# Kernel tuning notes

Measured on AMD Instinct MI355X. Metric: run time of the kernel, lower is better.

Reference implementation:

```python
import jax, jax.numpy as jnp
import numpy as np

E, H, D, T, B = 768, 12, 64, 2048, 2
HID = 4 * E

def _layernorm(x, g, b, eps=1e-5):
    mu = jnp.mean(x, axis=-1, keepdims=True)
    var = jnp.mean(jnp.square(x - mu), axis=-1, keepdims=True)
    return (x - mu) * jax.lax.rsqrt(var + eps) * g + b

def setup_inputs() -> dict:
    key = jax.random.key(0)
    ks = jax.random.split(key, 8)
    s = 0.02
    return {
        "x": jax.random.normal(ks[0], (B, T, E), jnp.float32),
        "Wq": jax.random.normal(ks[1], (H, E, D), jnp.float32) * s,
        "Wk": jax.random.normal(ks[2], (H, E, D), jnp.float32) * s,
        "Wv": jax.random.normal(ks[3], (H, E, D), jnp.float32) * s,
        "W1": jax.random.normal(ks[4], (E, HID), jnp.float32) * s,
        "b1": jnp.zeros((HID,), jnp.float32),
        "W2": jax.random.normal(ks[5], (HID, E), jnp.float32) * s,
        "b2": jnp.zeros((E,), jnp.float32),
        "ln1_g": jnp.ones((E,), jnp.float32),
        "ln1_b": jnp.zeros((E,), jnp.float32),
        "ln2_g": jnp.ones((E,), jnp.float32),
        "ln2_b": jnp.zeros((E,), jnp.float32),
    }

def reference(x, Wq, Wk, Wv, W1, b1, W2, b2, ln1_g, ln1_b, ln2_g, ln2_b):
    b, t, e = x.shape
    # per-head projections (stacked): [B,H,T,D]
    q = jnp.einsum('bte,hed->bhtd', x, Wq)
    k = jnp.einsum('bte,hed->bhtd', x, Wk)
    v = jnp.einsum('bte,hed->bhtd', x, Wv)
    scores = jnp.einsum('bhtd,bhsd->bhts', q, k) / jnp.sqrt(jnp.float32(D))
    causal = jnp.tril(jnp.ones((t, t), bool))
    masked = jnp.where(causal, scores, -jnp.inf)
    p = jax.nn.softmax(masked, axis=-1)
    av = jnp.einsum('bhts,bhsd->bhtd', p, v)  # [B,H,T,D]
    attn_out = av.transpose(0, 2, 1, 3).reshape(b, t, e)  # concat heads
    y = _layernorm(x + attn_out, ln1_g, ln1_b)
    mlp = jnp.maximum(y @ W1 + b1, 0.0) @ W2 + b2
    return _layernorm(y + mlp, ln2_g, ln2_b)
```

## Files before the change

kernel.cpp:

```cpp
#include <hip/hip_runtime.h>
#include <stdint.h>

constexpr int Ee   = 768;
constexpr int Hh   = 12;
constexpr int Dd   = 64;
constexpr int Tt   = 2048;
constexpr int Bb   = 2;
constexpr int HIDc = 3072;
constexpr int MROWS = Bb * Tt;
constexpr int NQKV  = 3 * Hh * Dd;

typedef unsigned short u16;
typedef __bf16 bf16;
typedef bf16 bf16x8 __attribute__((ext_vector_type(8)));
typedef float f32x4 __attribute__((ext_vector_type(4)));
typedef float f32x16 __attribute__((ext_vector_type(16)));

__device__ __forceinline__ u16 f2bf(float f) {
  uint32_t u = __builtin_bit_cast(uint32_t, f);
  u += 0x7fffu + ((u >> 16) & 1u);
  return (u16)(u >> 16);
}

__device__ __forceinline__ uint32_t cvt_pk_bf16(float lo, float hi) {
  uint32_t r;
  asm("v_cvt_pk_bf16_f32 %0, %1, %2" : "=v"(r) : "v"(lo), "v"(hi));
  return r;
}

__device__ __forceinline__ f32x4 mfma16(bf16x8 a, bf16x8 b, f32x4 c) {
  return __builtin_amdgcn_mfma_f32_16x16x32_bf16(a, b, c, 0, 0, 0);
}

__device__ __forceinline__ f32x16 mfma32(bf16x8 a, bf16x8 b, f32x16 c) {
  return __builtin_amdgcn_mfma_f32_32x32x16_bf16(a, b, c, 0, 0, 0);
}

#define GLOAD_LDS16(gp, lp)                                                            \
  __builtin_amdgcn_global_load_lds((const __attribute__((address_space(1))) void*)(gp),\
                                   (__attribute__((address_space(3))) void*)(lp),      \
                                   16, 0, 0)

#define KSWZ(row, byte) ((row) * 128 + ((byte) ^ (((row) & 7) << 4)))


__device__ __forceinline__ void tr_body(const float* __restrict__ ip,
                                        u16* __restrict__ op,
                                        int R, int C, int r0, int c0,
                                        float (*t)[33]) {
  const int tx = threadIdx.x & 31, ty = threadIdx.x >> 5;
#pragma unroll
  for (int i = 0; i < 4; ++i)
    t[ty * 4 + i][tx] = ip[(size_t)(r0 + ty * 4 + i) * C + c0 + tx];
  __syncthreads();
#pragma unroll
  for (int i = 0; i < 4; ++i)
    op[(size_t)(c0 + ty * 4 + i) * R + r0 + tx] = f2bf(t[tx][ty * 4 + i]);
}

__global__ __launch_bounds__(256) void prep_kernel(
    const float* __restrict__ x, u16* __restrict__ xb,
    const float* __restrict__ Wq, const float* __restrict__ Wk,
    const float* __restrict__ Wv, u16* __restrict__ wqkvt,
    const float* __restrict__ W1, u16* __restrict__ w1t,
    const float* __restrict__ W2, u16* __restrict__ w2t) {
  __shared__ float t[32][33];
  int bid = blockIdx.x;
  if (bid < 3072) {
    const int i = bid * 256 + threadIdx.x;
    const float4 f = *(const float4*)(x + (size_t)i * 4);
    uint2 o;
    u16* po = (u16*)&o;
    po[0] = f2bf(f.x); po[1] = f2bf(f.y); po[2] = f2bf(f.z); po[3] = f2bf(f.w);
    *(uint2*)(xb + (size_t)i * 4) = o;
    return;
  }
  bid -= 3072;
  if (bid < 1728) {
    const int bx = bid & 1;
    const int rest = bid >> 1;
    const int by = rest % 24, z = rest / 24;
    const int which = z / 12, hs = z - which * 12;
    const float* W = (which == 0) ? Wq : (which == 1) ? Wk : Wv;
    tr_body(W + (size_t)hs * Ee * Dd, wqkvt + ((size_t)which * 768 + hs * 64) * Ee,
            Ee, Dd, by * 32, bx * 32, t);
    return;
  }
  bid -= 1728;
  if (bid < 2304) {
    const int bx = bid % 96, by = bid / 96;
    tr_body(W1, w1t, Ee, HIDc, by * 32, bx * 32, t);
    return;
  }
  bid -= 2304;
  {
    const int bx = bid % 24, by = bid / 24;
    tr_body(W2, w2t, HIDc, Ee, by * 32, bx * 32, t);
  }
}

template <int EPI, int SPLITK>
__global__ __launch_bounds__(256, 4) void gemm_bt_kernel(
    const u16* __restrict__ A, const u16* __restrict__ Bt,
    const float* __restrict__ bias,
    u16* __restrict__ out_u, float* __restrict__ out_f,
    u16* __restrict__ qp, u16* __restrict__ kp, u16* __restrict__ vp,
    int Mdim, int Ndim, int Kdim, int gx, int gy) {
  __shared__ u16 la[3][128 * 32];
  __shared__ u16 lb[3][128 * 32];
  const int tid = threadIdx.x, lane = tid & 63, wv = tid >> 6;
  const int wm = wv >> 1, wn = wv & 1;
  const int l15 = lane & 15, l4 = lane >> 4;

  const int nwg = gx * gy * SPLITK;
  const int cpx = nwg >> 3;
  const int wg = (blockIdx.x & 7) * cpx + (blockIdx.x >> 3);
  const int bx = wg % gx;
  const int byz = wg / gx;
  const int by = byz % gy;
  const int kz = byz / gy;
  const int m0 = by * 128, n0 = bx * 128;
  const int Ks = Kdim / SPLITK;
  const int kbase = kz * Ks;
  const int niter = Ks / 32;

  auto stage = [&](int it, int buf) {
    const int k0 = kbase + it * 32;
#pragma unroll
    for (int j = 0; j < 2; ++j) {
      const int ci = j * 256 + tid;
      const int row = ci >> 2, sl = ci & 3;
      const int ke = (sl ^ ((row >> 1) & 3)) * 8;
      GLOAD_LDS16(A + (size_t)(m0 + row) * Kdim + k0 + ke, la[buf] + (size_t)ci * 8);
    }
#pragma unroll
    for (int j = 0; j < 2; ++j) {
      const int ci = j * 256 + tid;
      const int row = ci >> 2, sl = ci & 3;
      const int ke = (sl ^ ((row >> 1) & 3)) * 8;
      GLOAD_LDS16(Bt + (size_t)(n0 + row) * Kdim + k0 + ke, lb[buf] + (size_t)ci * 8);
    }
  };

  f32x4 acc[4][4] = {};

  auto compute = [&](int buf) {
    const char* lac = (const char*)la[buf];
    const char* lbc = (const char*)lb[buf];
    bf16x8 af[4], bfr[4];
#pragma unroll
    for (int i = 0; i < 4; ++i) {
      const int ra = wm * 64 + i * 16 + l15;
      af[i]  = *(const bf16x8*)(lac + ra * 64 + ((l4 * 16) ^ (((ra >> 1) & 3) << 4)));
      const int rb = wn * 64 + i * 16 + l15;
      bfr[i] = *(const bf16x8*)(lbc + rb * 64 + ((l4 * 16) ^ (((rb >> 1) & 3) << 4)));
    }
    __builtin_amdgcn_s_setprio(1);
#pragma unroll
    for (int mi = 0; mi < 4; ++mi)
#pragma unroll
      for (int ni = 0; ni < 4; ++ni)
        acc[mi][ni] = mfma16(af[mi], bfr[ni], acc[mi][ni]);
    __builtin_amdgcn_s_setprio(0);
  };

  stage(0, 0);
  stage(1, 1);

  for (int it = 0; it < niter - 1; ++it) {
    asm volatile("s_waitcnt vmcnt(4)" ::: "memory");
    __builtin_amdgcn_sched_barrier(0);
    __builtin_amdgcn_s_barrier();
    __builtin_amdgcn_sched_barrier(0);
    if (it + 2 < niter) stage(it + 2, (it + 2) % 3);
    compute(it % 3);
  }
  asm volatile("s_waitcnt vmcnt(0)" ::: "memory");
  __builtin_amdgcn_sched_barrier(0);
  __builtin_amdgcn_s_barrier();
  __builtin_amdgcn_sched_barrier(0);
  compute((niter - 1) % 3);

#pragma unroll
  for (int mi = 0; mi < 4; ++mi)
#pragma unroll
    for (int ni = 0; ni < 4; ++ni) {
      const int mb = m0 + wm * 64 + mi * 16 + l4 * 4;
      const int n = n0 + wn * 64 + ni * 16 + l15;
      if constexpr (EPI == 0) {
        const int b = mb >> 11, tb = mb & 2047;
        const int which = n / (Hh * Dd);
        const int nn = n - which * (Hh * Dd);
        const int h = nn >> 6, d = nn & 63;
        if (which == 2) {
          uint2 pw;
          pw.x = cvt_pk_bf16(acc[mi][ni][0], acc[mi][ni][1]);
          pw.y = cvt_pk_bf16(acc[mi][ni][2], acc[mi][ni][3]);
          const int tp = (tb & ~15) | ((tb & 4) << 1) | ((tb & 8) >> 1);
          *(uint2*)(vp + ((size_t)(b * Hh + h) * Dd + d) * Tt + tp) = pw;
        } else {
          u16* dst = (which == 0) ? qp : kp;
#pragma unroll
          for (int r = 0; r < 4; ++r)
            dst[((size_t)(b * Hh + h) * Tt + tb + r) * Dd + d] = f2bf(acc[mi][ni][r]);
        }
      } else if constexpr (EPI == 1) {
#pragma unroll
        for (int r = 0; r < 4; ++r) {
          float val = acc[mi][ni][r] + bias[n];
          val = fmaxf(val, 0.0f);
          out_u[(size_t)(mb + r) * Ndim + n] = f2bf(val);
        }
      } else {
#pragma unroll
        for (int r = 0; r < 4; ++r) {
          float val = acc[mi][ni][r];
          if (kz == 0) val += bias[n];
          out_f[(size_t)kz * Mdim * Ndim + (size_t)(mb + r) * Ndim + n] = val;
        }
      }
    }
}

__global__ __launch_bounds__(256) void attn_kernel(const u16* __restrict__ q,
                                                   const u16* __restrict__ k,
                                                   const u16* __restrict__ vtg,
                                                   float* __restrict__ Pb,
                                                   float* __restrict__ Lb) {
  __shared__ u16 kl[2][64 * 64];
  __shared__ u16 vt[2][64 * 64];
  const int tid = threadIdx.x, lane = tid & 63, w = tid >> 6;
  const int l31 = lane & 31, hi = lane >> 5;
  const int bid = blockIdx.x;
  const int x8 = bid & 7, r3 = bid >> 3;
  const int g = r3 % 3, u = r3 / 3;
  int q128, c, nt;
  if (u < 4)       { q128 = 15; c = u; nt = 8; }
  else if (u < 16) { const int v = u - 4;  q128 = 14 - v / 3; c = v % 3; nt = 8; }
  else if (u < 24) { const int v = u - 16; q128 = 10 - v / 2; c = v % 2; nt = 8; }
  else if (u < 28) { q128 = 6 - (u - 24); c = 0; nt = 8; }
  else             { const int v = u - 28; const int row = v >> 2, col = v & 3;
                     nt = 6 - 2 * row; q128 = 14 - row - 4 * col; c = 3 - col; }
  const int ts0 = c * 8;
  const int bh = g * 8 + x8;
  const int wq = 2 * q128 + (w >> 1);
  const int tg = q128 * 128 + (w >> 1) * 64 + (w & 1) * 32 + l31;
  constexpr float SC = 0.18033688f;

  const u16* kgb = k + (size_t)bh * Tt * Dd;
  const u16* vgb = vtg + (size_t)bh * Dd * Tt;

  bf16x8 qf[4];
#pragma unroll
  for (int kt = 0; kt < 4; ++kt)
    qf[kt] = *(const bf16x8*)(q + ((size_t)bh * Tt + tg) * Dd + kt * 16 + hi * 8);

  {
    const int sb0 = ts0 * 64;
#pragma unroll
    for (int jj = 0; jj < 2; ++jj) {
      const int cb = (w * 2 + jj) * 64;
      const int ci = cb + lane;
      const int row = ci >> 3;
      const int sb = ((ci & 7) * 16) ^ ((row & 7) << 4);
      GLOAD_LDS16(kgb + (size_t)(sb0 + row) * Dd + (sb >> 1), kl[0] + (size_t)cb * 8);
      GLOAD_LDS16(vgb + (size_t)row * Tt + sb0 + (sb >> 1), vt[0] + (size_t)cb * 8);
    }
  }

  f32x16 oacc0 = {}, oacc1 = {};
  float lrun = 0.f;

  for (int jt = 0; jt < nt; ++jt) {
    __syncthreads();
    const int cur = jt & 1;
    if (jt + 1 < nt) {
      const int s0n = (ts0 + jt + 1) * 64;
#pragma unroll
      for (int jj = 0; jj < 2; ++jj) {
        const int cb = (w * 2 + jj) * 64;
        const int ci = cb + lane;
        const int row = ci >> 3;
        const int sb = ((ci & 7) * 16) ^ ((row & 7) << 4);
        GLOAD_LDS16(kgb + (size_t)(s0n + row) * Dd + (sb >> 1), kl[cur ^ 1] + (size_t)cb * 8);
        GLOAD_LDS16(vgb + (size_t)row * Tt + s0n + (sb >> 1), vt[cur ^ 1] + (size_t)cb * 8);
      }
    }
    const int tile = ts0 + jt;
    if (tile <= wq) {
      const u16* klc = kl[cur];
      const u16* vtc = vt[cur];

      f32x16 sacc0 = {}, sacc1 = {};
      __builtin_amdgcn_s_setprio(1);
#pragma unroll
      for (int kt = 0; kt < 4; ++kt) {
        const int b0 = kt * 32 + hi * 16;
        const bf16x8 kf0 = *(const bf16x8*)((const char*)klc + KSWZ(l31, b0));
        const bf16x8 kf1 = *(const bf16x8*)((const char*)klc + KSWZ(32 + l31, b0));
        sacc0 = mfma32(kf0, qf[kt], sacc0);
        sacc1 = mfma32(kf1, qf[kt], sacc1);
      }
      __builtin_amdgcn_s_setprio(0);

      const bool diag = (tile == wq);
      bf16x8 pf[4];
      float rs = 0.f;
#pragma unroll
      for (int sh = 0; sh < 2; ++sh) {
        const f32x16 sa = sh ? sacc1 : sacc0;
#pragma unroll
        for (int kt2 = 0; kt2 < 2; ++kt2) {
          float p8[8];
#pragma unroll
          for (int o = 0; o < 8; ++o) {
            const int r = kt2 * 8 + o;
            float e = __builtin_amdgcn_exp2f(sa[r] * SC);
            if (diag) {
              const int sg = tile * 64 + sh * 32 + kt2 * 16 + (o & 3) + 8 * (o >> 2) + 4 * hi;
              e = (sg > tg) ? 0.f : e;
            }
            p8[o] = e;
            rs += e;
          }
          uint4 uu;
          uu.x = cvt_pk_bf16(p8[0], p8[1]);
          uu.y = cvt_pk_bf16(p8[2], p8[3]);
          uu.z = cvt_pk_bf16(p8[4], p8[5]);
          uu.w = cvt_pk_bf16(p8[6], p8[7]);
          pf[sh * 2 + kt2] = __builtin_bit_cast(bf16x8, uu);
        }
      }
      lrun += rs;

      __builtin_amdgcn_s_setprio(1);
#pragma unroll
      for (int ks = 0; ks < 4; ++ks) {
        const int b0 = ks * 32 + hi * 16;
        const bf16x8 vf0 = *(const bf16x8*)((const char*)vtc + KSWZ(l31, b0));
        const bf16x8 vf1 = *(const bf16x8*)((const char*)vtc + KSWZ(32 + l31, b0));
        oacc0 = mfma32(vf0, pf[ks], oacc0);
        oacc1 = mfma32(vf1, pf[ks], oacc1);
      }
      __builtin_amdgcn_s_setprio(0);
    }
  }

  const float lt = lrun + __shfl_xor(lrun, 32);
  const int b = bh / Hh, h = bh - (bh / Hh) * Hh;
  float* orow = Pb + (size_t)c * MROWS * Ee + ((size_t)b * Tt + tg) * Ee + h * Dd;
#pragma unroll
  for (int dt = 0; dt < 2; ++dt) {
    const f32x16 oa = dt ? oacc1 : oacc0;
#pragma unroll
    for (int kq = 0; kq < 4; ++kq) {
      float4 ov;
      ov.x = oa[4 * kq + 0];
      ov.y = oa[4 * kq + 1];
      ov.z = oa[4 * kq + 2];
      ov.w = oa[4 * kq + 3];
      *(float4*)(orow + dt * 32 + 8 * kq + 4 * hi) = ov;
    }
  }
  if (hi == 0)
    Lb[(size_t)c * MROWS * 12 + ((size_t)b * Tt + tg) * 12 + h] = lt;
}

__global__ __launch_bounds__(256) void ln1_kernel(const float* __restrict__ x,
                                                  const float* __restrict__ P,
                                                  const float* __restrict__ L,
                                                  const float* __restrict__ g,
                                                  const float* __restrict__ beta,
                                                  float* __restrict__ yout,
                                                  u16* __restrict__ ybout) {
  const int m = blockIdx.x;
  const int t = m & (Tt - 1);
  __shared__ float ls[12];
  __shared__ float rs[8], rss[8];
  if (threadIdx.x < 12) {
    float s = L[(size_t)m * 12 + threadIdx.x];
    if (t >= 512)  s += L[(size_t)1 * MROWS * 12 + (size_t)m * 12 + threadIdx.x];
    if (t >= 1024) s += L[(size_t)2 * MROWS * 12 + (size_t)m * 12 + threadIdx.x];
    if (t >= 1536) s += L[(size_t)3 * MROWS * 12 + (size_t)m * 12 + threadIdx.x];
    ls[threadIdx.x] = 1.0f / s;
  }
  __syncthreads();
  float vbuf[3];
  float s = 0.f, ss = 0.f;
#pragma unroll
  for (int i = 0; i < 3; ++i) {
    const int e = threadIdx.x + i * 256;
    float o = P[(size_t)m * Ee + e];
    if (t >= 512)  o += P[(size_t)1 * MROWS * Ee + (size_t)m * Ee + e];
    if (t >= 1024) o += P[(size_t)2 * MROWS * Ee + (size_t)m * Ee + e];
    if (t >= 1536) o += P[(size_t)3 * MROWS * Ee + (size_t)m * Ee + e];
    const float tv = x[(size_t)m * Ee + e] + o * ls[e >> 6];
    vbuf[i] = tv;
    s += tv;
    ss += tv * tv;
  }
#pragma unroll
  for (int off = 32; off; off >>= 1) {
    s += __shfl_xor(s, off);
    ss += __shfl_xor(ss, off);
  }
  const int wv = threadIdx.x >> 6, ln = threadIdx.x & 63;
  if (ln == 0) { rs[wv] = s; rss[wv] = ss; }
  __syncthreads();
  if (threadIdx.x == 0) {
    float S = 0.f, SS = 0.f;
    for (int i = 0; i < 4; ++i) { S += rs[i]; SS += rss[i]; }
    rs[4] = S; rss[4] = SS;
  }
  __syncthreads();
  const float mu = rs[4] / Ee;
  const float var = rss[4] / Ee - mu * mu;
  const float inv = rsqrtf(var + 1e-5f);
#pragma unroll
  for (int i = 0; i < 3; ++i) {
    const int e = threadIdx.x + i * 256;
    const float tv = (vbuf[i] - mu) * inv * g[e] + beta[e];
    yout[(size_t)m * Ee + e] = tv;
    ybout[(size_t)m * Ee + e] = f2bf(tv);
  }
}

__global__ __launch_bounds__(256) void ln2_kernel(const float* __restrict__ a,
                                                  const float* __restrict__ mlp,
                                                  const float* __restrict__ g,
                                                  const float* __restrict__ beta,
                                                  float* __restrict__ yout) {
  const int m = blockIdx.x;
  float vbuf[3];
  float s = 0.f, ss = 0.f;
#pragma unroll
  for (int i = 0; i < 3; ++i) {
    const int e = threadIdx.x + i * 256;
    float t = a[(size_t)m * Ee + e];
#pragma unroll
    for (int kz = 0; kz < 2; ++kz)
      t += mlp[(size_t)kz * MROWS * Ee + (size_t)m * Ee + e];
    vbuf[i] = t;
    s += t;
    ss += t * t;
  }
#pragma unroll
  for (int off = 32; off; off >>= 1) {
    s += __shfl_xor(s, off);
    ss += __shfl_xor(ss, off);
  }
  __shared__ float rs[8], rss[8];
  const int wv = threadIdx.x >> 6, ln = threadIdx.x & 63;
  if (ln == 0) { rs[wv] = s; rss[wv] = ss; }
  __syncthreads();
  if (threadIdx.x == 0) {
    float S = 0.f, SS = 0.f;
    for (int i = 0; i < 4; ++i) { S += rs[i]; SS += rss[i]; }
    rs[4] = S; rss[4] = SS;
  }
  __syncthreads();
  const float mu = rs[4] / Ee;
  const float var = rss[4] / Ee - mu * mu;
  const float inv = rsqrtf(var + 1e-5f);
#pragma unroll
  for (int i = 0; i < 3; ++i) {
    const int e = threadIdx.x + i * 256;
    yout[(size_t)m * Ee + e] = (vbuf[i] - mu) * inv * g[e] + beta[e];
  }
}

extern "C" void kernel_launch(void* const* d_in, const int* in_sizes, int n_in,
                              void* d_out, int out_size, void* d_ws, size_t ws_size,
                              hipStream_t stream) {
  const float* x  = (const float*)d_in[0];
  const float* Wq = (const float*)d_in[1];
  const float* Wk = (const float*)d_in[2];
  const float* Wv = (const float*)d_in[3];
  const float* W1 = (const float*)d_in[4];
  const float* b1 = (const float*)d_in[5];
  const float* W2 = (const float*)d_in[6];
  const float* b2 = (const float*)d_in[7];
  const float* g1 = (const float*)d_in[8];
  const float* be1 = (const float*)d_in[9];
  const float* g2 = (const float*)d_in[10];
  const float* be2 = (const float*)d_in[11];
  float* out = (float*)d_out;

  char* ws = (char*)d_ws;
  size_t off = 0;
  auto alloc = [&](size_t bytes) -> char* {
    char* p = ws + off;
    off += (bytes + 255) & ~(size_t)255;
    return p;
  };
  u16* xb    = (u16*)alloc((size_t)MROWS * Ee * 2);
  u16* wqkvt = (u16*)alloc((size_t)NQKV * Ee * 2);
  u16* w1t   = (u16*)alloc((size_t)HIDc * Ee * 2);
  u16* w2t   = (u16*)alloc((size_t)Ee * HIDc * 2);
  u16* qb    = (u16*)alloc((size_t)Bb * Hh * Tt * Dd * 2);
  u16* kb    = (u16*)alloc((size_t)Bb * Hh * Tt * Dd * 2);
  u16* vtb   = (u16*)alloc((size_t)Bb * Hh * Tt * Dd * 2);
  float* y    = (float*)alloc((size_t)MROWS * Ee * 4);
  u16* yb     = (u16*)alloc((size_t)MROWS * Ee * 2);
  float* Lb   = (float*)alloc((size_t)4 * MROWS * 12 * 4);
  char* big = alloc((size_t)MROWS * HIDc * 2 + (size_t)4 * MROWS * Ee * 4);
  float* Pb  = (float*)big;
  u16* hbuf  = (u16*)big;
  float* mlp = (float*)(big + (size_t)MROWS * HIDc * 2);
  (void)ws_size;

  prep_kernel<<<9408, 256, 0, stream>>>(x, xb, Wq, Wk, Wv, wqkvt, W1, w1t, W2, w2t);

  gemm_bt_kernel<0, 1><<<18 * 32, 256, 0, stream>>>(
      xb, wqkvt, nullptr, nullptr, nullptr, qb, kb, vtb, MROWS, NQKV, Ee, 18, 32);

  attn_kernel<<<960, 256, 0, stream>>>(qb, kb, vtb, Pb, Lb);

  ln1_kernel<<<MROWS, 256, 0, stream>>>(x, Pb, Lb, g1, be1, y, yb);

  gemm_bt_kernel<1, 1><<<24 * 32, 256, 0, stream>>>(
      yb, w1t, b1, hbuf, nullptr, nullptr, nullptr, nullptr, MROWS, HIDc, Ee, 24, 32);
  gemm_bt_kernel<2, 2><<<6 * 32 * 2, 256, 0, stream>>>(
      hbuf, w2t, b2, nullptr, mlp, nullptr, nullptr, nullptr, MROWS, Ee, HIDc, 6, 32);

  ln2_kernel<<<MROWS, 256, 0, stream>>>(y, mlp, g2, be2, out);
}
```

Baseline: 162.2 us.

## Use 256x128 GEMM tiles with 8 waves and store attention partials as bf16

The GEMM kernel now uses 512-thread blocks, each computing a 256x128 tile. This halves the grid and lets more waves share each B tile. The pipeline loop is restructured to issue the next stage before computing, with a single barrier per iteration. Separately, the attention partial outputs are written as bf16 instead of fp32 and converted back in ln1, which halves that traffic at some cost in precision. The workspace shrinks to match, and the smaller Pb still aliases hbuf.

Result: slower. 176.1 us (+8.6%).

```diff
diff --git a/kernel.cpp b/kernel.cpp
--- a/kernel.cpp
+++ b/kernel.cpp
@@ -20,6 +20,11 @@
   uint32_t u = __builtin_bit_cast(uint32_t, f);
   u += 0x7fffu + ((u >> 16) & 1u);
   return (u16)(u >> 16);
+}
+
+__device__ __forceinline__ float bf2f(u16 v) {
+  uint32_t u = (uint32_t)v << 16;
+  return __builtin_bit_cast(float, u);
 }
 
 __device__ __forceinline__ uint32_t cvt_pk_bf16(float lo, float hi) {
@@ -100,16 +105,16 @@
 }
 
 template <int EPI, int SPLITK>
-__global__ __launch_bounds__(256, 4) void gemm_bt_kernel(
+__global__ __launch_bounds__(512, 4) void gemm8_kernel(
     const u16* __restrict__ A, const u16* __restrict__ Bt,
     const float* __restrict__ bias,
     u16* __restrict__ out_u, float* __restrict__ out_f,
     u16* __restrict__ qp, u16* __restrict__ kp, u16* __restrict__ vp,
     int Mdim, int Ndim, int Kdim, int gx, int gy) {
-  __shared__ u16 la[3][128 * 32];
+  __shared__ u16 la[3][256 * 32];
   __shared__ u16 lb[3][128 * 32];
-  const int tid = threadIdx.x, lane = tid & 63, wv = tid >> 6;
-  const int wm = wv >> 1, wn = wv & 1;
+  const int tid = threadIdx.x, lane = tid & 63, wid = tid >> 6;
+  const int wm = wid >> 1, wn = wid & 1;
   const int l15 = lane & 15, l4 = lane >> 4;
 
   const int nwg = gx * gy * SPLITK;
@@ -119,34 +124,39 @@
   const int byz = wg / gx;
   const int by = byz % gy;
   const int kz = byz / gy;
-  const int m0 = by * 128, n0 = bx * 128;
+  const int m0 = by * 256, n0 = bx * 128;
   const int Ks = Kdim / SPLITK;
   const int kbase = kz * Ks;
   const int niter = Ks / 32;
 
-  auto stage = [&](int it, int buf) {
+  auto stage = [&](int it, int slot) {
     const int k0 = kbase + it * 32;
 #pragma unroll
     for (int j = 0; j < 2; ++j) {
-      const int ci = j * 256 + tid;
+      const int ci = j * 512 + tid;
       const int row = ci >> 2, sl = ci & 3;
       const int ke = (sl ^ ((row >> 1) & 3)) * 8;
-      GLOAD_LDS16(A + (size_t)(m0 + row) * Kdim + k0 + ke, la[buf] + (size_t)ci * 8);
-    }
-#pragma unroll
-    for (int j = 0; j < 2; ++j) {
-      const int ci = j * 256 + tid;
+      GLOAD_LDS16(A + (size_t)(m0 + row) * Kdim + k0 + ke, la[slot] + (size_t)ci * 8);
+    }
+    {
+      const int ci = tid;
       const int row = ci >> 2, sl = ci & 3;
       const int ke = (sl ^ ((row >> 1) & 3)) * 8;
-      GLOAD_LDS16(Bt + (size_t)(n0 + row) * Kdim + k0 + ke, lb[buf] + (size_t)ci * 8);
+      GLOAD_LDS16(Bt + (size_t)(n0 + row) * Kdim + k0 + ke, lb[slot] + (size_t)ci * 8);
     }
   };
 
   f32x4 acc[4][4] = {};
-
-  auto compute = [&](int buf) {
-    const char* lac = (const char*)la[buf];
-    const char* lbc = (const char*)lb[buf];
+  stage(0, 0);
+  stage(1, 1);
+  asm volatile("s_waitcnt vmcnt(3)" ::: "memory");
+  __builtin_amdgcn_s_barrier();
+
+  for (int it = 0; it < niter; ++it) {
+    const int slot = it % 3;
+    if (it + 2 < niter) stage(it + 2, (it + 2) % 3);
+    const char* lac = (const char*)la[slot];
+    const char* lbc = (const char*)lb[slot];
     bf16x8 af[4], bfr[4];
 #pragma unroll
     for (int i = 0; i < 4; ++i) {
@@ -162,24 +172,12 @@
       for (int ni = 0; ni < 4; ++ni)
         acc[mi][ni] = mfma16(af[mi], bfr[ni], acc[mi][ni]);
     __builtin_amdgcn_s_setprio(0);
-  };
-
-  stage(0, 0);
-  stage(1, 1);
-
-  for (int it = 0; it < niter - 1; ++it) {
-    asm volatile("s_waitcnt vmcnt(4)" ::: "memory");
-    __builtin_amdgcn_sched_barrier(0);
+    if (it + 2 < niter)
+      asm volatile("s_waitcnt vmcnt(3)" ::: "memory");
+    else
+      asm volatile("s_waitcnt vmcnt(0)" ::: "memory");
     __builtin_amdgcn_s_barrier();
-    __builtin_amdgcn_sched_barrier(0);
-    if (it + 2 < niter) stage(it + 2, (it + 2) % 3);
-    compute(it % 3);
-  }
-  asm volatile("s_waitcnt vmcnt(0)" ::: "memory");
-  __builtin_amdgcn_sched_barrier(0);
-  __builtin_amdgcn_s_barrier();
-  __builtin_amdgcn_sched_barrier(0);
-  compute((niter - 1) % 3);
+  }
 
 #pragma unroll
   for (int mi = 0; mi < 4; ++mi)
@@ -225,7 +223,7 @@
 __global__ __launch_bounds__(256) void attn_kernel(const u16* __restrict__ q,
                                                    const u16* __restrict__ k,
                                                    const u16* __restrict__ vtg,
-                                                   float* __restrict__ Pb,
+                                                   u16* __restrict__ Pb,
                                                    float* __restrict__ Lb) {
   __shared__ u16 kl[2][64 * 64];
   __shared__ u16 vt[2][64 * 64];
@@ -348,18 +346,16 @@
 
   const float lt = lrun + __shfl_xor(lrun, 32);
   const int b = bh / Hh, h = bh - (bh / Hh) * Hh;
-  float* orow = Pb + (size_t)c * MROWS * Ee + ((size_t)b * Tt + tg) * Ee + h * Dd;
+  u16* orow = Pb + (size_t)c * MROWS * Ee + ((size_t)b * Tt + tg) * Ee + h * Dd;
 #pragma unroll
   for (int dt = 0; dt < 2; ++dt) {
     const f32x16 oa = dt ? oacc1 : oacc0;
 #pragma unroll
     for (int kq = 0; kq < 4; ++kq) {
-      float4 ov;
-      ov.x = oa[4 * kq + 0];
-      ov.y = oa[4 * kq + 1];
-      ov.z = oa[4 * kq + 2];
-      ov.w = oa[4 * kq + 3];
-      *(float4*)(orow + dt * 32 + 8 * kq + 4 * hi) = ov;
+      uint2 pw;
+      pw.x = cvt_pk_bf16(oa[4 * kq + 0], oa[4 * kq + 1]);
+      pw.y = cvt_pk_bf16(oa[4 * kq + 2], oa[4 * kq + 3]);
+      *(uint2*)(orow + dt * 32 + 8 * kq + 4 * hi) = pw;
     }
   }
   if (hi == 0)
@@ -367,7 +363,7 @@
 }
 
 __global__ __launch_bounds__(256) void ln1_kernel(const float* __restrict__ x,
-                                                  const float* __restrict__ P,
+                                                  const u16* __restrict__ P,
                                                   const float* __restrict__ L,
                                                   const float* __restrict__ g,
                                                   const float* __restrict__ beta,
@@ -390,10 +386,10 @@
 #pragma unroll
   for (int i = 0; i < 3; ++i) {
     const int e = threadIdx.x + i * 256;
-    float o = P[(size_t)m * Ee + e];
-    if (t >= 512)  o += P[(size_t)1 * MROWS * Ee + (size_t)m * Ee + e];
-    if (t >= 1024) o += P[(size_t)2 * MROWS * Ee + (size_t)m * Ee + e];
-    if (t >= 1536) o += P[(size_t)3 * MROWS * Ee + (size_t)m * Ee + e];
+    float o = bf2f(P[(size_t)m * Ee + e]);
+    if (t >= 512)  o += bf2f(P[(size_t)1 * MROWS * Ee + (size_t)m * Ee + e]);
+    if (t >= 1024) o += bf2f(P[(size_t)2 * MROWS * Ee + (size_t)m * Ee + e]);
+    if (t >= 1536) o += bf2f(P[(size_t)3 * MROWS * Ee + (size_t)m * Ee + e]);
     const float tv = x[(size_t)m * Ee + e] + o * ls[e >> 6];
     vbuf[i] = tv;
     s += tv;
@@ -503,25 +499,25 @@
   float* y    = (float*)alloc((size_t)MROWS * Ee * 4);
   u16* yb     = (u16*)alloc((size_t)MROWS * Ee * 2);
   float* Lb   = (float*)alloc((size_t)4 * MROWS * 12 * 4);
-  char* big = alloc((size_t)MROWS * HIDc * 2 + (size_t)4 * MROWS * Ee * 4);
-  float* Pb  = (float*)big;
+  char* big = alloc((size_t)MROWS * HIDc * 2 + (size_t)2 * MROWS * Ee * 4);
+  u16* Pb    = (u16*)big;
   u16* hbuf  = (u16*)big;
   float* mlp = (float*)(big + (size_t)MROWS * HIDc * 2);
   (void)ws_size;
 
   prep_kernel<<<9408, 256, 0, stream>>>(x, xb, Wq, Wk, Wv, wqkvt, W1, w1t, W2, w2t);
 
-  gemm_bt_kernel<0, 1><<<18 * 32, 256, 0, stream>>>(
-      xb, wqkvt, nullptr, nullptr, nullptr, qb, kb, vtb, MROWS, NQKV, Ee, 18, 32);
+  gemm8_kernel<0, 1><<<18 * 16, 512, 0, stream>>>(
+      xb, wqkvt, nullptr, nullptr, nullptr, qb, kb, vtb, MROWS, NQKV, Ee, 18, 16);
 
   attn_kernel<<<960, 256, 0, stream>>>(qb, kb, vtb, Pb, Lb);
 
   ln1_kernel<<<MROWS, 256, 0, stream>>>(x, Pb, Lb, g1, be1, y, yb);
 
-  gemm_bt_kernel<1, 1><<<24 * 32, 256, 0, stream>>>(
-      yb, w1t, b1, hbuf, nullptr, nullptr, nullptr, nullptr, MROWS, HIDc, Ee, 24, 32);
-  gemm_bt_kernel<2, 2><<<6 * 32 * 2, 256, 0, stream>>>(
-      hbuf, w2t, b2, nullptr, mlp, nullptr, nullptr, nullptr, MROWS, Ee, HIDc, 6, 32);
+  gemm8_kernel<1, 1><<<24 * 16, 512, 0, stream>>>(
+      yb, w1t, b1, hbuf, nullptr, nullptr, nullptr, nullptr, MROWS, HIDc, Ee, 24, 16);
+  gemm8_kernel<2, 2><<<6 * 16 * 2, 512, 0, stream>>>(
+      hbuf, w2t, b2, nullptr, mlp, nullptr, nullptr, nullptr, MROWS, Ee, HIDc, 6, 16);
 
   ln2_kernel<<<MROWS, 256, 0, stream>>>(y, mlp, g2, be2, out);
 }
```
